# Kernel optimization log

Hardware: AMD Instinct MI355X
Metric: run time of the kernel (lower is better)

## Reference

```python
import jax, jax.numpy as jnp
import numpy as np

TAU = 0.25    # membrane decay
GAMA = 1.0    # surrogate-gradient width

@jax.custom_vjp
def zif(u):
    # Heaviside spike with rectangular surrogate gradient (ZIF)
    return (u > 0).astype(u.dtype)

def _zif_fwd(u):
    return zif(u), u

def _zif_bwd(u, g):
    tmp = (1.0 / (GAMA * GAMA)) * jnp.clip(GAMA - jnp.abs(u), 0.0)
    return (g * tmp,)

zif.defvjp(_zif_fwd, _zif_bwd)


def setup_inputs() -> dict:
    key = jax.random.key(0)
    k1, _ = jax.random.split(key)
    x = jax.random.normal(k1, (32, 16, 65536), dtype=jnp.float32)  # [B, T, N]
    thresh = jnp.ones((1,), dtype=jnp.float32)                     # learnable threshold
    return {"x": x, "thresh": thresh}


def reference(x, thresh):
    # x: [B, T, N]; sequential LIF recurrence over T via lax.scan
    xT = jnp.moveaxis(x, 1, 0)  # [T, B, N]

    def step(mem, xt):
        mem = mem * TAU + xt                 # decay + integrate
        spike = zif(mem - thresh)            # threshold spike
        mem = (1.0 - spike) * mem            # multiplicative reset
        return mem, spike

    mem0 = jnp.zeros_like(xT[0])
    _, spikes = jax.lax.scan(step, mem0, xT)  # spikes: [T, B, N]
    return jnp.moveaxis(spikes, 0, 1)         # [B, T, N]
```

## Files before the change

### kernel.cpp

```cpp
#include <hip/hip_runtime.h>


#define TAU 0.25f

typedef float f32x4 __attribute__((ext_vector_type(4)));

__global__ __launch_bounds__(256) void lif_fwd_kernel(
    const float* __restrict__ x,
    const float* __restrict__ thresh,
    float* __restrict__ out)
{
    constexpr int T    = 16;
    constexpr int N    = 65536;
    constexpr int TILE = 1024;

    __shared__ float lds[T * TILE];

    const int tid  = threadIdx.x;
    const int wave = tid >> 6;
    const int lane = tid & 63;

    const int tile_idx = blockIdx.x & 63;
    const int b        = blockIdx.x >> 6;

    const size_t row0 = (size_t)b * T * N + (size_t)tile_idx * TILE;

#pragma unroll
    for (int t = 0; t < T; ++t) {
        const float* gsrc = x + row0 + (size_t)t * N + wave * 256 + lane * 4;
        float*       ldst = lds + t * TILE + wave * 256;
        __builtin_amdgcn_global_load_lds(
            (const __attribute__((address_space(1))) void*)gsrc,
            (__attribute__((address_space(3))) void*)ldst,
            16, 0, 0);
    }

    asm volatile("s_waitcnt vmcnt(0)" ::: "memory");
    __builtin_amdgcn_sched_barrier(0);

    const float th  = thresh[0];
    const int   col = tid * 4;

    f32x4 mem = {0.f, 0.f, 0.f, 0.f};

#pragma unroll
    for (int t = 0; t < T; ++t) {
        f32x4 xt = *(const f32x4*)(lds + t * TILE + col);

        mem.x = mem.x * TAU + xt.x;
        mem.y = mem.y * TAU + xt.y;
        mem.z = mem.z * TAU + xt.z;
        mem.w = mem.w * TAU + xt.w;

        const bool px = mem.x > th;
        const bool py = mem.y > th;
        const bool pz = mem.z > th;
        const bool pw = mem.w > th;

        f32x4 s;
        s.x = px ? 1.f : 0.f;
        s.y = py ? 1.f : 0.f;
        s.z = pz ? 1.f : 0.f;
        s.w = pw ? 1.f : 0.f;

        mem.x = px ? 0.f : mem.x;
        mem.y = py ? 0.f : mem.y;
        mem.z = pz ? 0.f : mem.z;
        mem.w = pw ? 0.f : mem.w;

        __builtin_nontemporal_store(s, (f32x4*)(out + row0 + (size_t)t * N + col));
    }
}

extern "C" void kernel_launch(void* const* d_in, const int* in_sizes, int n_in,
                              void* d_out, int out_size, void* d_ws, size_t ws_size,
                              hipStream_t stream)
{
    const float* x      = (const float*)d_in[0];
    const float* thresh = (const float*)d_in[1];
    float*       out    = (float*)d_out;

    const int total = in_sizes[0];
    const int grid  = total / (16 * 1024);
    const int block = 256;

    lif_fwd_kernel<<<grid, block, 0, stream>>>(x, thresh, out);
}
```

Measured before the change: 231.2 us.

## Double-buffer LDS staging across persistent chunks per block

Each block now handles eight 512-column chunks in sequence, using two LDS buffers. The next chunk is loaded with global_load_lds while the current one is computed. The grid shrinks by four times, and the per-lane load width drops from 16 bytes to 4 bytes, with two loads per wave per time step. The goal is to overlap load latency with compute and stores, at the cost of more load instructions and fewer blocks in flight.

```diff
diff --git a/kernel.cpp b/kernel.cpp
--- a/kernel.cpp
+++ b/kernel.cpp
@@ -3,72 +3,88 @@
 
 #define TAU 0.25f
 
-typedef float f32x4 __attribute__((ext_vector_type(4)));
+typedef float f32x2 __attribute__((ext_vector_type(2)));
+
+__device__ __forceinline__ void stage_chunk(
+    const float* __restrict__ gbase,
+    float* __restrict__ lbase,
+    int w, int lane)
+{
+    constexpr int N = 65536;
+#pragma unroll
+    for (int t = 0; t < 16; ++t) {
+#pragma unroll
+        for (int h = 0; h < 2; ++h) {
+            const float* gsrc = gbase + (size_t)t * N + w * 128 + h * 64 + lane;
+            float*       ldst = lbase + t * 512 + w * 128 + h * 64;
+            __builtin_amdgcn_global_load_lds(
+                (const __attribute__((address_space(1))) void*)gsrc,
+                (__attribute__((address_space(3))) void*)ldst,
+                4, 0, 0);
+        }
+    }
+}
 
 __global__ __launch_bounds__(256) void lif_fwd_kernel(
     const float* __restrict__ x,
     const float* __restrict__ thresh,
     float* __restrict__ out)
 {
-    constexpr int T    = 16;
-    constexpr int N    = 65536;
-    constexpr int TILE = 1024;
+    constexpr int T      = 16;
+    constexpr int N      = 65536;
+    constexpr int TILE   = 512;
+    constexpr int CHUNKS = 8;
 
-    __shared__ float lds[T * TILE];
+    __shared__ float lds[2][T][TILE];
 
     const int tid  = threadIdx.x;
-    const int wave = tid >> 6;
+    const int w    = tid >> 6;
     const int lane = tid & 63;
 
-    const int tile_idx = blockIdx.x & 63;
-    const int b        = blockIdx.x >> 6;
+    const int b  = blockIdx.x >> 4;
+    const int nb = blockIdx.x & 15;
+    const size_t xbase = (size_t)b * T * N + (size_t)nb * (CHUNKS * TILE);
 
-    const size_t row0 = (size_t)b * T * N + (size_t)tile_idx * TILE;
+    const float th  = thresh[0];
+    const int   col = w * 128 + lane * 2;
+
+    stage_chunk(x + xbase, &lds[0][0][0], w, lane);
+
+    for (int c = 0; c < CHUNKS; ++c) {
+        const int buf = c & 1;
+
+        if (c + 1 < CHUNKS) {
+            stage_chunk(x + xbase + (size_t)(c + 1) * TILE,
+                        &lds[buf ^ 1][0][0], w, lane);
+            asm volatile("s_waitcnt vmcnt(32)" ::: "memory");
+        } else {
+            asm volatile("s_waitcnt vmcnt(0)" ::: "memory");
+        }
+        __builtin_amdgcn_sched_barrier(0);
+
+        float mx = 0.f, my = 0.f;
+        const float* lp = &lds[buf][0][0];
+        float*       gp = out + xbase + (size_t)c * TILE;
 
 #pragma unroll
-    for (int t = 0; t < T; ++t) {
-        const float* gsrc = x + row0 + (size_t)t * N + wave * 256 + lane * 4;
-        float*       ldst = lds + t * TILE + wave * 256;
-        __builtin_amdgcn_global_load_lds(
-            (const __attribute__((address_space(1))) void*)gsrc,
-            (__attribute__((address_space(3))) void*)ldst,
-            16, 0, 0);
-    }
+        for (int t = 0; t < T; ++t) {
+            f32x2 xt = *(const f32x2*)(lp + t * TILE + col);
 
-    asm volatile("s_waitcnt vmcnt(0)" ::: "memory");
-    __builtin_amdgcn_sched_barrier(0);
+            mx = mx * TAU + xt.x;
+            my = my * TAU + xt.y;
 
-    const float th  = thresh[0];
-    const int   col = tid * 4;
+            const bool px = mx > th;
+            const bool py = my > th;
 
-    f32x4 mem = {0.f, 0.f, 0.f, 0.f};
+            f32x2 s;
+            s.x = px ? 1.f : 0.f;
+            s.y = py ? 1.f : 0.f;
 
-#pragma unroll
-    for (int t = 0; t < T; ++t) {
-        f32x4 xt = *(const f32x4*)(lds + t * TILE + col);
+            mx = px ? 0.f : mx;
+            my = py ? 0.f : my;
 
-        mem.x = mem.x * TAU + xt.x;
-        mem.y = mem.y * TAU + xt.y;
-        mem.z = mem.z * TAU + xt.z;
-        mem.w = mem.w * TAU + xt.w;
-
-        const bool px = mem.x > th;
-        const bool py = mem.y > th;
-        const bool pz = mem.z > th;
-        const bool pw = mem.w > th;
-
-        f32x4 s;
-        s.x = px ? 1.f : 0.f;
-        s.y = py ? 1.f : 0.f;
-        s.z = pz ? 1.f : 0.f;
-        s.w = pw ? 1.f : 0.f;
-
-        mem.x = px ? 0.f : mem.x;
-        mem.y = py ? 0.f : mem.y;
-        mem.z = pz ? 0.f : mem.z;
-        mem.w = pw ? 0.f : mem.w;
-
-        __builtin_nontemporal_store(s, (f32x4*)(out + row0 + (size_t)t * N + col));
+            __builtin_nontemporal_store(s, (f32x2*)(gp + (size_t)t * N + col));
+        }
     }
 }
 
@@ -81,7 +97,7 @@
     float*       out    = (float*)d_out;
 
     const int total = in_sizes[0];
-    const int grid  = total / (16 * 1024);
+    const int grid  = total / (16 * 4096);
     const int block = 256;
 
     lif_fwd_kernel<<<grid, block, 0, stream>>>(x, thresh, out);
```

Measured after the change: 248.3 us. +7.4%, slower.
